# Kernel tuning notes

Hardware: AMD Instinct MI355X
Metric: run time of the kernel (lower is better)

The kernel has to match this reference:

```python
import jax, jax.numpy as jnp
import numpy as np

K = 30  # hardcoded top-k in take_top_k_dropout(x, 30, ...)


def _topk_channel_mask(x, k):
    # x: [B, C, H, W]; binary mask with 1 at the top-k |x| channels per pixel.
    B, C, H, W = x.shape
    xa = jnp.abs(x).reshape(B, C, H * W).transpose(0, 2, 1).reshape(B * H * W, C)
    _, idx = jax.lax.top_k(xa, k)  # [BHW, k]
    rows = jnp.arange(B * H * W)[:, None]
    mask = jnp.zeros((B * H * W, C), x.dtype).at[rows, idx].set(1.0)
    return mask.reshape(B, H * W, C).transpose(0, 2, 1).reshape(B, C, H, W)


def _saturation(z, phi, jump):
    # Saturation_activation_per_filter.forward
    l1 = (jnp.sum(jnp.abs(phi), axis=0) + 1e-12).reshape(1, -1, 1, 1)  # [1,C,1,1]
    r = z / l1
    r = 0.5 * (jnp.sign(r - jump) + jnp.sign(r + jump))
    return r * l1


def _conv_transpose(x, w, b, stride):
    # PyTorch ConvTranspose2d(padding=0): w is [in, out, kh, kw]
    k = w.shape[-1]
    wt = jnp.flip(w, (2, 3)).transpose(1, 0, 2, 3)  # -> [out, in, kh, kw]
    y = jax.lax.conv_general_dilated(
        x, wt, window_strides=(1, 1),
        padding=[(k - 1, k - 1), (k - 1, k - 1)],
        lhs_dilation=(stride, stride),
        dimension_numbers=('NCHW', 'OIHW', 'NCHW'))
    return y + b.reshape(1, -1, 1, 1)


def _take_middle(x):
    width = x.shape[-1]
    s = (width - 32) // 2
    return x[:, :, s:s + 32, s:s + 32]


def setup_inputs() -> dict:
    key = jax.random.key(0)
    ks = jax.random.split(key, 9)
    B, C, H, W, D = 128, 500, 16, 16, 192
    return {
        'x': jax.random.normal(ks[0], (B, C, H, W), jnp.float32),
        'phi': jax.random.normal(ks[1], (D, C), jnp.float32),
        'jump': jnp.float32(0.1),
        'w1': jax.random.normal(ks[2], (C, 300, 4, 4), jnp.float32) * 0.02,
        'b1': jax.random.normal(ks[3], (300,), jnp.float32) * 0.02,
        'w2': jax.random.normal(ks[4], (300, 100, 3, 3), jnp.float32) * 0.02,
        'b2': jax.random.normal(ks[5], (100,), jnp.float32) * 0.02,
        'w3': jax.random.normal(ks[6], (100, 3, 3, 3), jnp.float32) * 0.02,
        'b3': jax.random.normal(ks[7], (3,), jnp.float32) * 0.02,
    }


def reference(x, phi, jump, w1, b1, w2, b2, w3, b3):
    # eval mode: dropout(ones) == ones, no training rescalings
    out = x * _topk_channel_mask(x, K)
    out = _saturation(out, phi, jump)
    out = jax.nn.relu(_conv_transpose(out, w1, b1, 2))
    out = jax.nn.relu(_conv_transpose(out, w2, b2, 1))
    out = jax.nn.relu(_conv_transpose(out, w3, b3, 1))
    return _take_middle(out)
```

## Files before the change

kernel.cpp:

```cpp
#include <hip/hip_runtime.h>
#include <stdint.h>

#define B_   128
#define C_   500
#define H_   16
#define P_   256
#define D_   192
#define C1O  300
#define H1   34
#define P1   (H1*H1)
#define C2O  100
#define H2   36
#define P2   (H2*H2)
#define C3O  3
#define H3   38
#define P3   (H3*H3)
#define CROP 3
#define OW_  32
#define KTOP 30

#define NL1B   16
#define NZQBLK (B_ * 4)
#define NB3BLK ((P3 + 3) / 4)

__device__ __forceinline__ float sgnf(float v){ return (v > 0.f) ? 1.f : ((v < 0.f) ? -1.f : 0.f); }

__device__ __forceinline__ int pat36(int i){
  if (i == 0) return 0;
  if (i == 1) return 1;
  if (i <= 33) return 2;
  if (i == 34) return 3;
  return 4;
}

__global__ void k_setup(const float* __restrict__ phi, const float* __restrict__ jumpp,
                        const float* __restrict__ w2, const float* __restrict__ b1,
                        const float* __restrict__ b2,
                        float* __restrict__ l1, float* __restrict__ thr,
                        float* __restrict__ tab){
  const int blk = blockIdx.x;
  const int t = threadIdx.x;

  if (blk < NL1B){
    __shared__ float red[8][32];
    const int cl = t & 31, dg = t >> 5;
    const int c = blk * 32 + cl;
    float s = 0.f;
    if (c < C_){
      const int d0 = dg * 24;
#pragma unroll 4
      for (int d = d0; d < d0 + 24; ++d) s += fabsf(phi[d * C_ + c]);
    }
    red[dg][cl] = s;
    __syncthreads();
    if (t < 32){
      int cc = blk * 32 + t;
      if (cc < C_){
        float sum = 1e-12f;
#pragma unroll
        for (int g = 0; g < 8; ++g) sum += red[g][t];
        l1[cc] = sum;
        thr[cc] = jumpp[0] * sum;
      }
    }
    return;
  }

  __shared__ float S[9];
  const int o = blk - NL1B;
  if (t < 64){
    float acc[9] = {0,0,0,0,0,0,0,0,0};
    for (int c = t; c < C1O; c += 64){
      float a1 = fmaxf(b1[c], 0.f);
      const float* w = w2 + (c * C2O + o) * 9;
#pragma unroll
      for (int tap = 0; tap < 9; ++tap) acc[tap] += w[tap] * a1;
    }
#pragma unroll
    for (int tap = 0; tap < 9; ++tap)
      for (int off = 32; off; off >>= 1) acc[tap] += __shfl_down(acc[tap], off);
    if (t == 0){
#pragma unroll
      for (int tap = 0; tap < 9; ++tap) S[tap] = acc[tap];
    }
  }
  __syncthreads();
  if (t < 25){
    const int lo[5] = {0,0,0,1,2}, hi[5] = {0,1,2,2,2};
    int pr = t / 5, pc = t % 5;
    float s = b2[o];
    for (int kh = lo[pr]; kh <= hi[pr]; ++kh)
      for (int kw = lo[pc]; kw <= hi[pc]; ++kw) s += S[kh * 3 + kw];
    tab[o * 25 + t] = s;
  }
}

__global__ void k_scan_b3(const float* __restrict__ x, const float* __restrict__ thr,
                          const float* __restrict__ tab, const float* __restrict__ w3,
                          const float* __restrict__ b3,
                          unsigned char* __restrict__ d0, float* __restrict__ base3){
  if (blockIdx.x >= NZQBLK){
    const int wave = threadIdx.x >> 6, lane = threadIdx.x & 63;
    const int pix = (blockIdx.x - NZQBLK) * 4 + wave;
    if (pix >= P3) return;
    const int oh = pix / H3, ow = pix % H3;
    float acc[3] = {0, 0, 0};
    for (int c = lane; c < C2O; c += 64){
      const float* w = w3 + c * 27;
#pragma unroll
      for (int kh = 0; kh < 3; ++kh){
        int ih = oh - kh; if (ih < 0 || ih >= H2) continue;
        int prr = pat36(ih) * 5;
#pragma unroll
        for (int kw = 0; kw < 3; ++kw){
          int iw = ow - kw; if (iw < 0 || iw >= H2) continue;
          float a2 = fmaxf(tab[c * 25 + prr + pat36(iw)], 0.f);
#pragma unroll
          for (int o = 0; o < 3; ++o) acc[o] += w[o * 9 + kh * 3 + kw] * a2;
        }
      }
    }
#pragma unroll
    for (int o = 0; o < 3; ++o){
      for (int off = 32; off; off >>= 1) acc[o] += __shfl_down(acc[o], off);
    }
    if (lane == 0){
#pragma unroll
      for (int o = 0; o < 3; ++o) base3[o * P3 + pix] = acc[o] + b3[o];
    }
    return;
  }

  const int b = blockIdx.x >> 2;
  const int tile = (blockIdx.x & 3) * 64;
  const int t = threadIdx.x;
  const int q = t & 15, cg = t >> 4;

  __shared__ unsigned char um[256];

  unsigned m = 0;
  const int pbase = tile + 4 * q;
  for (int c = cg; c < C_; c += 16){
    float tc = thr[c];
    const float4 v = *(const float4*)(x + ((size_t)(b * C_ + c)) * P_ + pbase);
    if (fabsf(v.x) >= tc) m |= 1u;
    if (fabsf(v.y) >= tc) m |= 2u;
    if (fabsf(v.z) >= tc) m |= 4u;
    if (fabsf(v.w) >= tc) m |= 8u;
  }
  um[t] = (unsigned char)m;
  __syncthreads();
  if (t < 64){
    const int qq = t >> 2, j = t & 3;
    unsigned mm = 0;
#pragma unroll
    for (int g = 0; g < 16; ++g) mm |= um[g * 16 + qq];
    d0[b * P_ + tile + t] = (unsigned char)((mm >> j) & 1u);
  }
}

__global__ void k_final(const float* __restrict__ x, const float* __restrict__ l1,
                        const float* __restrict__ jumpp, const float* __restrict__ tab,
                        const float* __restrict__ w1, const float* __restrict__ b1,
                        const float* __restrict__ w2, const float* __restrict__ w3,
                        const float* __restrict__ base3, const unsigned char* __restrict__ d0,
                        signed char* __restrict__ zq, float* __restrict__ u1,
                        float* __restrict__ u2, float* __restrict__ out, int have){
  const int b = blockIdx.x;
  const int t = threadIdx.x;
  const int wave = t >> 6, lane = t & 63;

  __shared__ unsigned char hot[P_];
  __shared__ unsigned char d1s[P1];
  __shared__ unsigned char d2s[P2];
  __shared__ int s_any;
  __shared__ float sx[C_];
  __shared__ unsigned char rm[C_];
  __shared__ unsigned long long red[4];
  __shared__ int sel[KTOP];

  hot[t] = d0[b * P_ + t];
  if (t == 0) s_any = 0;
  __syncthreads();
  if (hot[t]) s_any = 1;
  __syncthreads();

  if (!s_any){
    for (int i = t; i < 3 * OW_ * (OW_ / 4); i += 256){
      int o = i >> 8, rr = i & 255;
      int r = rr >> 3, q4 = rr & 7;
      int oh = r + CROP, ow0 = q4 * 4 + CROP;
      const float* bp = base3 + o * P3 + oh * H3 + ow0;
      float4 res;
      res.x = fmaxf(bp[0], 0.f);
      res.y = fmaxf(bp[1], 0.f);
      res.z = fmaxf(bp[2], 0.f);
      res.w = fmaxf(bp[3], 0.f);
      *(float4*)(out + ((size_t)(b * 3 + o) * OW_ + r) * OW_ + q4 * 4) = res;
    }
    return;
  }
  if (!have) return;

  const float J = jumpp[0];

  for (int px = 0; px < P_; ++px){
    if (!hot[px]) continue;
    for (int c = t; c < C_; c += 256){ sx[c] = x[(b * C_ + c) * P_ + px]; rm[c] = 0; }
    __syncthreads();
    for (int it = 0; it < KTOP; ++it){
      unsigned long long best = 0ULL;
      for (int c = t; c < C_; c += 256){
        if (!rm[c]){
          unsigned long long key =
            ((unsigned long long)__float_as_uint(fabsf(sx[c])) << 32) |
            (unsigned int)(C_ - 1 - c);
          if (key > best) best = key;
        }
      }
      for (int off = 32; off; off >>= 1){
        unsigned long long o2 = __shfl_down(best, off);
        if (o2 > best) best = o2;
      }
      if ((t & 63) == 0) red[t >> 6] = best;
      __syncthreads();
      if (t == 0){
        unsigned long long mx = red[0];
        for (int wv = 1; wv < 4; ++wv) if (red[wv] > mx) mx = red[wv];
        int idx = C_ - 1 - (int)(mx & 0xffffffffULL);
        sel[it] = idx;
        rm[idx] = 1;
      }
      __syncthreads();
    }
    for (int c = t; c < C_; c += 256) zq[(b * C_ + c) * P_ + px] = 0;
    __syncthreads();
    if (t < KTOP){
      int c = sel[t];
      float r = sx[c] / l1[c];
      float qv = 0.5f * (sgnf(r - J) + sgnf(r + J));
      int code = (int)(2.f * qv);
      if (code) zq[(b * C_ + c) * P_ + px] = (signed char)code;
    }
    __syncthreads();
  }

  for (int p1 = t; p1 < P1; p1 += 256){
    int ih = p1 / H1, iw = p1 - (p1 / H1) * H1;
    int h0 = max(0, (ih - 2) >> 1), h1v = min(H_ - 1, ih >> 1);
    int w0 = max(0, (iw - 2) >> 1), w1v = min(H_ - 1, iw >> 1);
    int any = 0;
    for (int h = h0; h <= h1v; ++h)
      for (int w = w0; w <= w1v; ++w)
        any |= hot[h * H_ + w];
    d1s[p1] = (unsigned char)(any != 0);
  }
  __syncthreads();

  for (int p2 = t; p2 < P2; p2 += 256){
    int oh = p2 / H2, ow = p2 - (p2 / H2) * H2;
    int any = 0;
    for (int kh = 0; kh < 3; ++kh){
      int ih = oh - kh; if (ih < 0 || ih >= H1) continue;
      for (int kw = 0; kw < 3; ++kw){
        int iw = ow - kw; if (iw < 0 || iw >= H1) continue;
        any |= d1s[ih * H1 + iw];
      }
    }
    d2s[p2] = (unsigned char)(any != 0);
  }
  __syncthreads();

  for (int p1 = wave; p1 < P1; p1 += 4){
    if (!d1s[p1]) continue;
    int ih = p1 / H1, iw = p1 - (p1 / H1) * H1;
    float acc[5] = {0,0,0,0,0};
    int h0 = max(0, (ih - 2) >> 1), h1v = min(H_ - 1, ih >> 1);
    int w0 = max(0, (iw - 2) >> 1), w1v = min(H_ - 1, iw >> 1);
    for (int h = h0; h <= h1v; ++h)
      for (int w = w0; w <= w1v; ++w){
        if (!hot[h * H_ + w]) continue;
        int kh = ih - 2 * h, kw = iw - 2 * w;
        const signed char* zp = zq + (size_t)(b * C_) * P_ + h * H_ + w;
        for (int c = 0; c < C_; ++c){
          int code = zp[(size_t)c * P_];
          if (!code) continue;
          float val = 0.5f * (float)code * l1[c];
          const float* wp = w1 + (size_t)(c * C1O) * 16 + kh * 4 + kw;
#pragma unroll
          for (int j = 0; j < 5; ++j){
            int c1 = j * 64 + lane;
            if (c1 < C1O) acc[j] += wp[(size_t)c1 * 16] * val;
          }
        }
      }
#pragma unroll
    for (int j = 0; j < 5; ++j){
      int c1 = j * 64 + lane;
      if (c1 < C1O){
        float bb = b1[c1];
        u1[(size_t)(b * C1O + c1) * P1 + p1] = fmaxf(bb + acc[j], 0.f) - fmaxf(bb, 0.f);
      }
    }
  }
  __syncthreads();

  for (int p2 = wave; p2 < P2; p2 += 4){
    if (!d2s[p2]) continue;
    int oh = p2 / H2, ow = p2 - (p2 / H2) * H2;
    float acc[2] = {0,0};
    for (int kh = 0; kh < 3; ++kh){
      int ih = oh - kh; if (ih < 0 || ih >= H1) continue;
      for (int kw = 0; kw < 3; ++kw){
        int iw = ow - kw; if (iw < 0 || iw >= H1) continue;
        if (!d1s[ih * H1 + iw]) continue;
        const float* up = u1 + (size_t)(b * C1O) * P1 + ih * H1 + iw;
        const float* wb = w2 + kh * 3 + kw;
        for (int c1 = 0; c1 < C1O; ++c1){
          float uv = up[(size_t)c1 * P1];
          if (uv == 0.f) continue;
          const float* wp = wb + (size_t)(c1 * C2O) * 9;
#pragma unroll
          for (int j = 0; j < 2; ++j){
            int c2 = j * 64 + lane;
            if (c2 < C2O) acc[j] += wp[(size_t)c2 * 9] * uv;
          }
        }
      }
    }
    int pr = pat36(oh) * 5 + pat36(ow);
#pragma unroll
    for (int j = 0; j < 2; ++j){
      int c2 = j * 64 + lane;
      if (c2 < C2O){
        float bs = tab[c2 * 25 + pr];
        u2[(size_t)(b * C2O + c2) * P2 + p2] = fmaxf(bs + acc[j], 0.f) - fmaxf(bs, 0.f);
      }
    }
  }
  __syncthreads();

  for (int i = t; i < 3 * OW_ * OW_; i += 256){
    int o = i >> 10, rc = i & 1023;
    int r = rc >> 5, cc = rc & 31;
    int oh = r + CROP, ow = cc + CROP;
    float acc = base3[o * P3 + oh * H3 + ow];
    for (int kh = 0; kh < 3; ++kh){
      int ih = oh - kh;
      for (int kw = 0; kw < 3; ++kw){
        int iw = ow - kw;
        if (!d2s[ih * H2 + iw]) continue;
        const float* up = u2 + (size_t)(b * C2O) * P2 + ih * H2 + iw;
        const float* wp = w3 + o * 9 + kh * 3 + kw;
        for (int c2 = 0; c2 < C2O; ++c2){
          float uv = up[(size_t)c2 * P2];
          if (uv != 0.f) acc += wp[c2 * 27] * uv;
        }
      }
    }
    out[((size_t)(b * 3 + o) * OW_ + r) * OW_ + cc] = fmaxf(acc, 0.f);
  }
}

extern "C" void kernel_launch(void* const* d_in, const int* in_sizes, int n_in,
                              void* d_out, int out_size, void* d_ws, size_t ws_size,
                              hipStream_t stream){
  const float* x   = (const float*)d_in[0];
  const float* phi = (const float*)d_in[1];
  const float* jmp = (const float*)d_in[2];
  const float* w1  = (const float*)d_in[3];
  const float* b1  = (const float*)d_in[4];
  const float* w2  = (const float*)d_in[5];
  const float* b2  = (const float*)d_in[6];
  const float* w3  = (const float*)d_in[7];
  const float* b3  = (const float*)d_in[8];
  float* out = (float*)d_out;
  char* ws = (char*)d_ws;

  constexpr size_t OFF_L1  = 0;
  constexpr size_t OFF_THR = OFF_L1  + 2048;
  constexpr size_t OFF_TAB = OFF_THR + 2048;
  constexpr size_t OFF_B3  = OFF_TAB + 10240;
  constexpr size_t OFF_D0  = OFF_B3  + 17344;
  constexpr size_t OFF_ZQ  = OFF_D0  + (size_t)B_ * P_;
  constexpr size_t OFF_U1  = OFF_ZQ  + (size_t)B_ * C_ * P_;
  constexpr size_t OFF_U2  = OFF_U1  + (size_t)B_ * C1O * P1 * 4;
  constexpr size_t TOTAL   = OFF_U2  + (size_t)B_ * C2O * P2 * 4;

  float* l1p  = (float*)(ws + OFF_L1);
  float* thrp = (float*)(ws + OFF_THR);
  float* tabp = (float*)(ws + OFF_TAB);
  float* b3p  = (float*)(ws + OFF_B3);
  unsigned char* d0p = (unsigned char*)(ws + OFF_D0);
  signed char* zqp = (signed char*)(ws + OFF_ZQ);
  float* u1p = (float*)(ws + OFF_U1);
  float* u2p = (float*)(ws + OFF_U2);
  int have = (ws_size >= TOTAL) ? 1 : 0;

  k_setup  <<<NL1B + 100, 256, 0, stream>>>(phi, jmp, w2, b1, b2, l1p, thrp, tabp);
  k_scan_b3<<<NZQBLK + NB3BLK, 256, 0, stream>>>(x, thrp, tabp, w3, b3, d0p, b3p);
  k_final  <<<B_, 256, 0, stream>>>(x, l1p, jmp, tabp, w1, b1, w2, w3,
                                    b3p, d0p, zqp, u1p, u2p, out, have);
}
```

Measured before the change: 130.0 us.

## Decouple x scan from threshold via per-channel max, pack tab blocks

New measurement: 121.2 us. 6.7% less time.

```diff
diff --git a/kernel.cpp b/kernel.cpp
--- a/kernel.cpp
+++ b/kernel.cpp
@@ -20,8 +20,10 @@
 #define KTOP 30
 
 #define NL1B   16
-#define NZQBLK (B_ * 4)
-#define NB3BLK ((P3 + 3) / 4)
+#define NTABB  25
+#define NB3    361
+#define NSCAN  1000
+#define NPAIR  (B_ * C_)
 
 __device__ __forceinline__ float sgnf(float v){ return (v > 0.f) ? 1.f : ((v < 0.f) ? -1.f : 0.f); }
 
@@ -66,42 +68,42 @@
     return;
   }
 
-  __shared__ float S[9];
-  const int o = blk - NL1B;
-  if (t < 64){
-    float acc[9] = {0,0,0,0,0,0,0,0,0};
-    for (int c = t; c < C1O; c += 64){
-      float a1 = fmaxf(b1[c], 0.f);
-      const float* w = w2 + (c * C2O + o) * 9;
-#pragma unroll
-      for (int tap = 0; tap < 9; ++tap) acc[tap] += w[tap] * a1;
-    }
-#pragma unroll
-    for (int tap = 0; tap < 9; ++tap)
-      for (int off = 32; off; off >>= 1) acc[tap] += __shfl_down(acc[tap], off);
-    if (t == 0){
-#pragma unroll
-      for (int tap = 0; tap < 9; ++tap) S[tap] = acc[tap];
-    }
-  }
-  __syncthreads();
-  if (t < 25){
+  __shared__ float S[4][9];
+  const int wave = t >> 6, lane = t & 63;
+  const int o = (blk - NL1B) * 4 + wave;
+  float acc[9] = {0,0,0,0,0,0,0,0,0};
+  for (int c = lane; c < C1O; c += 64){
+    float a1 = fmaxf(b1[c], 0.f);
+    const float* w = w2 + (c * C2O + o) * 9;
+#pragma unroll
+    for (int tap = 0; tap < 9; ++tap) acc[tap] += w[tap] * a1;
+  }
+#pragma unroll
+  for (int tap = 0; tap < 9; ++tap)
+    for (int off = 32; off; off >>= 1) acc[tap] += __shfl_down(acc[tap], off);
+  if (lane == 0){
+#pragma unroll
+    for (int tap = 0; tap < 9; ++tap) S[wave][tap] = acc[tap];
+  }
+  __syncthreads();
+  if (lane < 25){
     const int lo[5] = {0,0,0,1,2}, hi[5] = {0,1,2,2,2};
-    int pr = t / 5, pc = t % 5;
+    int pr = lane / 5, pc = lane % 5;
     float s = b2[o];
     for (int kh = lo[pr]; kh <= hi[pr]; ++kh)
-      for (int kw = lo[pc]; kw <= hi[pc]; ++kw) s += S[kh * 3 + kw];
-    tab[o * 25 + t] = s;
+      for (int kw = lo[pc]; kw <= hi[pc]; ++kw) s += S[wave][kh * 3 + kw];
+    tab[o * 25 + lane] = s;
   }
 }
 
-__global__ void k_scan_b3(const float* __restrict__ x, const float* __restrict__ thr,
-                          const float* __restrict__ tab, const float* __restrict__ w3,
-                          const float* __restrict__ b3,
-                          unsigned char* __restrict__ d0, float* __restrict__ base3){
-  if (blockIdx.x >= NZQBLK){
-    const int wave = threadIdx.x >> 6, lane = threadIdx.x & 63;
-    const int pix = (blockIdx.x - NZQBLK) * 4 + wave;
+__global__ void k_scan_b3(const float* __restrict__ x, const float* __restrict__ tab,
+                          const float* __restrict__ w3, const float* __restrict__ b3,
+                          float* __restrict__ M, float* __restrict__ base3){
+  const int blk = blockIdx.x;
+  const int wave = threadIdx.x >> 6, lane = threadIdx.x & 63;
+
+  if (blk < NB3){
+    const int pix = blk * 4 + wave;
     if (pix >= P3) return;
     const int oh = pix / H3, ow = pix % H3;
     float acc[3] = {0, 0, 0};
@@ -131,31 +133,27 @@
     return;
   }
 
-  const int b = blockIdx.x >> 2;
-  const int tile = (blockIdx.x & 3) * 64;
-  const int t = threadIdx.x;
-  const int q = t & 15, cg = t >> 4;
-
-  __shared__ unsigned char um[256];
-
-  unsigned m = 0;
-  const int pbase = tile + 4 * q;
-  for (int c = cg; c < C_; c += 16){
-    float tc = thr[c];
-    const float4 v = *(const float4*)(x + ((size_t)(b * C_ + c)) * P_ + pbase);
-    if (fabsf(v.x) >= tc) m |= 1u;
-    if (fabsf(v.y) >= tc) m |= 2u;
-    if (fabsf(v.z) >= tc) m |= 4u;
-    if (fabsf(v.w) >= tc) m |= 8u;
-  }
-  um[t] = (unsigned char)m;
-  __syncthreads();
-  if (t < 64){
-    const int qq = t >> 2, j = t & 3;
-    unsigned mm = 0;
-#pragma unroll
-    for (int g = 0; g < 16; ++g) mm |= um[g * 16 + qq];
-    d0[b * P_ + tile + t] = (unsigned char)((mm >> j) & 1u);
+  const int g = (blk - NB3) * 4 + wave;
+  const float* xg = x + (size_t)g * 16 * P_ + lane * 4;
+#pragma unroll
+  for (int j0 = 0; j0 < 16; j0 += 4){
+    float4 v0 = *(const float4*)(xg + (size_t)(j0 + 0) * P_);
+    float4 v1 = *(const float4*)(xg + (size_t)(j0 + 1) * P_);
+    float4 v2 = *(const float4*)(xg + (size_t)(j0 + 2) * P_);
+    float4 v3 = *(const float4*)(xg + (size_t)(j0 + 3) * P_);
+    float m0 = fmaxf(fmaxf(fabsf(v0.x), fabsf(v0.y)), fmaxf(fabsf(v0.z), fabsf(v0.w)));
+    float m1 = fmaxf(fmaxf(fabsf(v1.x), fabsf(v1.y)), fmaxf(fabsf(v1.z), fabsf(v1.w)));
+    float m2 = fmaxf(fmaxf(fabsf(v2.x), fabsf(v2.y)), fmaxf(fabsf(v2.z), fabsf(v2.w)));
+    float m3 = fmaxf(fmaxf(fabsf(v3.x), fabsf(v3.y)), fmaxf(fabsf(v3.z), fabsf(v3.w)));
+#pragma unroll
+    for (int off = 32; off; off >>= 1){
+      m0 = fmaxf(m0, __shfl_down(m0, off));
+      m1 = fmaxf(m1, __shfl_down(m1, off));
+      m2 = fmaxf(m2, __shfl_down(m2, off));
+      m3 = fmaxf(m3, __shfl_down(m3, off));
+    }
+    if (lane == 0)
+      *(float4*)(M + g * 16 + j0) = make_float4(m0, m1, m2, m3);
   }
 }
 
@@ -163,7 +161,8 @@
                         const float* __restrict__ jumpp, const float* __restrict__ tab,
                         const float* __restrict__ w1, const float* __restrict__ b1,
                         const float* __restrict__ w2, const float* __restrict__ w3,
-                        const float* __restrict__ base3, const unsigned char* __restrict__ d0,
+                        const float* __restrict__ base3, const float* __restrict__ M,
+                        const float* __restrict__ thr,
                         signed char* __restrict__ zq, float* __restrict__ u1,
                         float* __restrict__ u2, float* __restrict__ out, int have){
   const int b = blockIdx.x;
@@ -171,6 +170,7 @@
   const int wave = t >> 6, lane = t & 63;
 
   __shared__ unsigned char hot[P_];
+  __shared__ unsigned char um[256];
   __shared__ unsigned char d1s[P1];
   __shared__ unsigned char d2s[P2];
   __shared__ int s_any;
@@ -179,10 +179,10 @@
   __shared__ unsigned long long red[4];
   __shared__ int sel[KTOP];
 
-  hot[t] = d0[b * P_ + t];
   if (t == 0) s_any = 0;
   __syncthreads();
-  if (hot[t]) s_any = 1;
+  for (int c = t; c < C_; c += 256)
+    if (M[b * C_ + c] >= thr[c]) s_any = 1;
   __syncthreads();
 
   if (!s_any){
@@ -201,6 +201,32 @@
     return;
   }
   if (!have) return;
+
+  {
+    const int q = t & 15, cg = t >> 4;
+    for (int tile = 0; tile < 4; ++tile){
+      unsigned m = 0;
+      const int pbase = tile * 64 + 4 * q;
+      for (int c = cg; c < C_; c += 16){
+        float tc = thr[c];
+        const float4 v = *(const float4*)(x + ((size_t)(b * C_ + c)) * P_ + pbase);
+        if (fabsf(v.x) >= tc) m |= 1u;
+        if (fabsf(v.y) >= tc) m |= 2u;
+        if (fabsf(v.z) >= tc) m |= 4u;
+        if (fabsf(v.w) >= tc) m |= 8u;
+      }
+      um[t] = (unsigned char)m;
+      __syncthreads();
+      if (t < 64){
+        const int qq = t >> 2, j = t & 3;
+        unsigned mm = 0;
+#pragma unroll
+        for (int g = 0; g < 16; ++g) mm |= um[g * 16 + qq];
+        hot[tile * 64 + t] = (unsigned char)((mm >> j) & 1u);
+      }
+      __syncthreads();
+    }
+  }
 
   const float J = jumpp[0];
 
@@ -381,8 +407,8 @@
   constexpr size_t OFF_THR = OFF_L1  + 2048;
   constexpr size_t OFF_TAB = OFF_THR + 2048;
   constexpr size_t OFF_B3  = OFF_TAB + 10240;
-  constexpr size_t OFF_D0  = OFF_B3  + 17344;
-  constexpr size_t OFF_ZQ  = OFF_D0  + (size_t)B_ * P_;
+  constexpr size_t OFF_M   = OFF_B3  + 17344;
+  constexpr size_t OFF_ZQ  = OFF_M   + (size_t)NPAIR * 4;
   constexpr size_t OFF_U1  = OFF_ZQ  + (size_t)B_ * C_ * P_;
   constexpr size_t OFF_U2  = OFF_U1  + (size_t)B_ * C1O * P1 * 4;
   constexpr size_t TOTAL   = OFF_U2  + (size_t)B_ * C2O * P2 * 4;
@@ -391,14 +417,14 @@
   float* thrp = (float*)(ws + OFF_THR);
   float* tabp = (float*)(ws + OFF_TAB);
   float* b3p  = (float*)(ws + OFF_B3);
-  unsigned char* d0p = (unsigned char*)(ws + OFF_D0);
+  float* Mp   = (float*)(ws + OFF_M);
   signed char* zqp = (signed char*)(ws + OFF_ZQ);
   float* u1p = (float*)(ws + OFF_U1);
   float* u2p = (float*)(ws + OFF_U2);
   int have = (ws_size >= TOTAL) ? 1 : 0;
 
-  k_setup  <<<NL1B + 100, 256, 0, stream>>>(phi, jmp, w2, b1, b2, l1p, thrp, tabp);
-  k_scan_b3<<<NZQBLK + NB3BLK, 256, 0, stream>>>(x, thrp, tabp, w3, b3, d0p, b3p);
+  k_setup  <<<NL1B + NTABB, 256, 0, stream>>>(phi, jmp, w2, b1, b2, l1p, thrp, tabp);
+  k_scan_b3<<<NB3 + NSCAN, 256, 0, stream>>>(x, tabp, w3, b3, Mp, b3p);
   k_final  <<<B_, 256, 0, stream>>>(x, l1p, jmp, tabp, w1, b1, w2, w3,
-                                    b3p, d0p, zqp, u1p, u2p, out, have);
+                                    b3p, Mp, thrp, zqp, u1p, u2p, out, have);
 }
```
